# Performance work log

Hardware: AMD Instinct MI355X
Metric: run time of the kernel (lower is better)

The kernel has to match this reference:

```python
import jax, jax.numpy as jnp
import numpy as np

B, S, D = 2, 2048, 1024
H = 16
HD = D // H


def setup_inputs() -> dict:
    key = jax.random.key(0)
    k1, k2, k3 = jax.random.split(key, 3)
    x = jax.random.normal(k1, (B, S, D), dtype=jnp.float32)
    # nn.Linear(d, 3d, bias=False): weight [3d, d]; y = x @ W.T
    w_qkv = jax.random.normal(k2, (3 * D, D), dtype=jnp.float32) * (D ** -0.5)
    w_out = jax.random.normal(k3, (D, D), dtype=jnp.float32) * (D ** -0.5)
    return {"x": x, "w_qkv": w_qkv, "w_out": w_out}


def reference(x, w_qkv, w_out):
    batch, seq_len, _ = x.shape
    qkv = jnp.einsum('bsd,ed->bse', x, w_qkv)  # [B,S,3D]
    q, k, v = jnp.split(qkv, 3, axis=-1)
    # [B,S,D] -> [B,H,S,HD]
    def heads(t):
        return t.reshape(batch, seq_len, H, HD).transpose(0, 2, 1, 3)
    q, k, v = heads(q), heads(k), heads(v)
    scale = HD ** -0.5
    attn = jnp.einsum('bhqd,bhkd->bhqk', q, k) * scale  # [B,H,S,S]
    causal = jnp.triu(jnp.ones((seq_len, seq_len), dtype=bool), k=1)
    attn = jnp.where(causal, -jnp.inf, attn)
    attn = jax.nn.softmax(attn, axis=-1)
    out = jnp.einsum('bhqk,bhkd->bhqd', attn, v)  # [B,H,S,HD]
    out = out.transpose(0, 2, 1, 3).reshape(batch, seq_len, D)
    return jnp.einsum('bsd,ed->bse', out, w_out)
```

## Files before the change

### kernel.cpp

```cpp
#include <hip/hip_runtime.h>

#define NUM_B 2
#define SEQ   2048
#define DIM   1024
#define NH    16
#define HD    64

typedef __attribute__((ext_vector_type(8))) short short8;
typedef __attribute__((ext_vector_type(4))) float floatx4;
typedef unsigned short us;

#define SOFTMAX_SHIFT 12.0f

__device__ __forceinline__ us f2bf(float f) {
    unsigned u = __float_as_uint(f);
    u += 0x7fffu + ((u >> 16) & 1u);
    return (us)(u >> 16);
}
__device__ __forceinline__ us f2bf_t(float f) {
    return (us)(__float_as_uint(f) >> 16);
}

#define GLD16(gptr, lptr) __builtin_amdgcn_global_load_lds( \
    (__attribute__((address_space(1))) unsigned int*)(gptr), \
    (__attribute__((address_space(3))) unsigned int*)(lptr), 16, 0, 0)

#define SETP(p) __builtin_amdgcn_s_setprio(p)

__global__ __launch_bounds__(256) void cast_all(
    const float* __restrict__ x, const float* __restrict__ wq,
    const float* __restrict__ wo, us* __restrict__ xb,
    us* __restrict__ wqb, us* __restrict__ wob)
{
    int i = blockIdx.x * 256 + threadIdx.x;
    const float* src; us* dst; int off;
    if (i < 524288)      { src = x;  dst = xb;  off = i; }
    else if (i < 917504) { src = wq; dst = wqb; off = i - 524288; }
    else                 { src = wo; dst = wob; off = i - 917504; }
    const float4* p = (const float4*)src + (size_t)off * 2;
    float4 f0 = p[0];
    float4 f1 = p[1];
    short8 v;
    v[0] = (short)f2bf(f0.x); v[1] = (short)f2bf(f0.y);
    v[2] = (short)f2bf(f0.z); v[3] = (short)f2bf(f0.w);
    v[4] = (short)f2bf(f1.x); v[5] = (short)f2bf(f1.y);
    v[6] = (short)f2bf(f1.z); v[7] = (short)f2bf(f1.w);
    *(short8*)(dst + (size_t)off * 8) = v;
}

__global__ __launch_bounds__(256, 2) void gemm_qkv(
    const us* __restrict__ A, const us* __restrict__ Bw,
    us* __restrict__ qb, us* __restrict__ kb, us* __restrict__ vt)
{
    __shared__ us As[128 * 64];
    __shared__ us Bs[128 * 64];
    const int t = threadIdx.x;
    const int lane = t & 63, w = t >> 6;
    const int l16 = lane & 15, quad = lane >> 4;
    const int wr = (w >> 1) * 64, wc = (w & 1) * 64;
    const int m0 = blockIdx.y * 128, n0 = blockIdx.x * 128;
    const bool isV = (blockIdx.x >= 16);
    const int srow = lane >> 3;
    const int soff = ((lane & 7) ^ srow) << 3;
    const int rsw  = l16 & 7;

    floatx4 acc[4][4];
    #pragma unroll
    for (int i = 0; i < 4; ++i)
        #pragma unroll
        for (int j = 0; j < 4; ++j) acc[i][j] = (floatx4){0.f, 0.f, 0.f, 0.f};

    for (int k0 = 0; k0 < DIM; k0 += 64) {
        #pragma unroll
        for (int c = 0; c < 4; ++c) {
            int chunk = w * 4 + c;
            int row = chunk * 8 + srow;
            GLD16(A  + (size_t)(m0 + row) * DIM + k0 + soff, &As[chunk * 512]);
            GLD16(Bw + (size_t)(n0 + row) * DIM + k0 + soff, &Bs[chunk * 512]);
        }
        __syncthreads();
        #pragma unroll
        for (int s = 0; s < 2; ++s) {
            short8 af[4], bf[4];
            #pragma unroll
            for (int i = 0; i < 4; ++i)
                af[i] = *(const short8*)&As[(wr + i * 16 + l16) * 64 + (((s * 4 + quad) ^ rsw) << 3)];
            #pragma unroll
            for (int j = 0; j < 4; ++j)
                bf[j] = *(const short8*)&Bs[(wc + j * 16 + l16) * 64 + (((s * 4 + quad) ^ rsw) << 3)];
            if (!isV) {
                #pragma unroll
                for (int i = 0; i < 4; ++i)
                    #pragma unroll
                    for (int j = 0; j < 4; ++j)
                        acc[i][j] = __builtin_amdgcn_mfma_f32_16x16x32_bf16(af[i], bf[j], acc[i][j], 0, 0, 0);
            } else {
                #pragma unroll
                for (int i = 0; i < 4; ++i)
                    #pragma unroll
                    for (int j = 0; j < 4; ++j)
                        acc[i][j] = __builtin_amdgcn_mfma_f32_16x16x32_bf16(bf[j], af[i], acc[i][j], 0, 0, 0);
            }
        }
        __syncthreads();
    }

    if (!isV) {
        const int which = n0 >> 10;
        const float sc = (which == 0) ? 0.125f : 1.0f;
        us* dst = (which == 0) ? qb : kb;
        #pragma unroll
        for (int i = 0; i < 4; ++i) {
            #pragma unroll
            for (int j = 0; j < 4; ++j) {
                int e = n0 + wc + j * 16 + l16;
                int h  = (e >> 6) & 15;
                int hd = e & 63;
                #pragma unroll
                for (int r = 0; r < 4; ++r) {
                    int m = m0 + wr + i * 16 + quad * 4 + r;
                    int b = m >> 11, s = m & 2047;
                    dst[((size_t)((b * NH + h) * SEQ + s) << 6) + hd] = f2bf(acc[i][j][r] * sc);
                }
            }
        }
    } else {
        #pragma unroll
        for (int i = 0; i < 4; ++i) {
            int m = m0 + wr + i * 16 + l16;
            int b = m >> 11, s = m & 2047;
            #pragma unroll
            for (int j = 0; j < 4; ++j) {
                int e0 = (n0 - 2048) + wc + j * 16 + quad * 4;
                #pragma unroll
                for (int r = 0; r < 4; ++r) {
                    int e = e0 + r;
                    int h = e >> 6, hd = e & 63;
                    vt[((size_t)((b * NH + h) * HD + hd) << 11) + s] = f2bf(acc[i][j][r]);
                }
            }
        }
    }
}

__global__ __launch_bounds__(256, 2) void gemm_out(
    const us* __restrict__ A, const us* __restrict__ Bw, float* __restrict__ outp)
{
    __shared__ us As[64 * 64];
    __shared__ us Bs[128 * 64];
    const int t = threadIdx.x;
    const int lane = t & 63, w = t >> 6;
    const int l16 = lane & 15, quad = lane >> 4;
    const int wr = (w >> 1) * 32, wc = (w & 1) * 64;
    const int m0 = blockIdx.y * 64, n0 = blockIdx.x * 128;
    const int srow = lane >> 3;
    const int soff = ((lane & 7) ^ srow) << 3;
    const int rsw  = l16 & 7;

    floatx4 acc[2][4];
    #pragma unroll
    for (int i = 0; i < 2; ++i)
        #pragma unroll
        for (int j = 0; j < 4; ++j) acc[i][j] = (floatx4){0.f, 0.f, 0.f, 0.f};

    for (int k0 = 0; k0 < DIM; k0 += 64) {
        #pragma unroll
        for (int c = 0; c < 2; ++c) {
            int chunk = w * 2 + c;
            int row = chunk * 8 + srow;
            GLD16(A + (size_t)(m0 + row) * DIM + k0 + soff, &As[chunk * 512]);
        }
        #pragma unroll
        for (int c = 0; c < 4; ++c) {
            int chunk = w * 4 + c;
            int row = chunk * 8 + srow;
            GLD16(Bw + (size_t)(n0 + row) * DIM + k0 + soff, &Bs[chunk * 512]);
        }
        __syncthreads();
        #pragma unroll
        for (int s = 0; s < 2; ++s) {
            short8 af[2], bf[4];
            #pragma unroll
            for (int i = 0; i < 2; ++i)
                af[i] = *(const short8*)&As[(wr + i * 16 + l16) * 64 + (((s * 4 + quad) ^ rsw) << 3)];
            #pragma unroll
            for (int j = 0; j < 4; ++j)
                bf[j] = *(const short8*)&Bs[(wc + j * 16 + l16) * 64 + (((s * 4 + quad) ^ rsw) << 3)];
            #pragma unroll
            for (int i = 0; i < 2; ++i)
                #pragma unroll
                for (int j = 0; j < 4; ++j)
                    acc[i][j] = __builtin_amdgcn_mfma_f32_16x16x32_bf16(af[i], bf[j], acc[i][j], 0, 0, 0);
        }
        __syncthreads();
    }

    #pragma unroll
    for (int i = 0; i < 2; ++i)
        #pragma unroll
        for (int j = 0; j < 4; ++j) {
            int n = n0 + wc + j * 16 + l16;
            #pragma unroll
            for (int r = 0; r < 4; ++r) {
                int m = m0 + wr + i * 16 + quad * 4 + r;
                outp[(size_t)m * DIM + n] = acc[i][j][r];
            }
        }
}

__global__ __launch_bounds__(256, 4) void attn(
    const us* __restrict__ qb, const us* __restrict__ kb,
    const us* __restrict__ vt, us* __restrict__ ob)
{
    __shared__ us Ks[2][64 * 64];
    __shared__ us Vs[2][64 * 64];
    __shared__ us Ps[4 * 16 * 72];
    const int t = threadIdx.x;
    const int lane = t & 63, w = t >> 6;
    const int l16 = lane & 15, quad = lane >> 4;
    const int idx = blockIdx.x;
    const int xcd   = idx & 7;
    const int local = idx >> 3;
    const int bh = (xcd << 2) | (local & 3);
    const int qt = 31 - (local >> 2);
    const int b = bh >> 4, h = bh & 15;
    const int q0 = qt << 6;
    const int r0 = q0 + w * 16;
    const int rowb = r0 + quad * 4;
    const size_t base = (size_t)bh * SEQ * HD;
    const us* qbh = qb + base;
    const us* kbh = kb + base;
    const us* vth = vt + base;
    us* Pp = Ps + w * 16 * 72;
    const int srow = lane >> 3;
    const int soff = ((lane & 7) ^ srow) << 3;
    const int rsw  = l16 & 7;

    short8 qa[2];
    #pragma unroll
    for (int s = 0; s < 2; ++s)
        qa[s] = *(const short8*)(qbh + (size_t)(r0 + l16) * HD + s * 32 + quad * 8);

    floatx4 o[4];
    #pragma unroll
    for (int j = 0; j < 4; ++j) o[j] = (floatx4){0.f, 0.f, 0.f, 0.f};
    float lrow[4] = {0.f, 0.f, 0.f, 0.f};

    #pragma unroll
    for (int c = 0; c < 2; ++c) {
        int chunk = w * 2 + c;
        int row = chunk * 8 + srow;
        GLD16(kbh + (size_t)row * HD + soff, &Ks[0][chunk * 512]);
        GLD16(vth + (size_t)row * SEQ + soff, &Vs[0][chunk * 512]);
    }
    __syncthreads();

    for (int kt = 0; kt <= qt; ++kt) {
        const int cur = kt & 1;
        if (kt < qt) {
            const int j0n = (kt + 1) << 6;
            #pragma unroll
            for (int c = 0; c < 2; ++c) {
                int chunk = w * 2 + c;
                int row = chunk * 8 + srow;
                GLD16(kbh + (size_t)(j0n + row) * HD + soff, &Ks[cur ^ 1][chunk * 512]);
                GLD16(vth + (size_t)row * SEQ + j0n + soff, &Vs[cur ^ 1][chunk * 512]);
            }
        }

        floatx4 sf[4];
        #pragma unroll
        for (int j = 0; j < 4; ++j)
            sf[j] = (floatx4){-SOFTMAX_SHIFT, -SOFTMAX_SHIFT, -SOFTMAX_SHIFT, -SOFTMAX_SHIFT};
        SETP(1);
        #pragma unroll
        for (int s = 0; s < 2; ++s)
            #pragma unroll
            for (int j = 0; j < 4; ++j) {
                short8 kf = *(const short8*)&Ks[cur][(j * 16 + l16) * 64 + (((s * 4 + quad) ^ rsw) << 3)];
                sf[j] = __builtin_amdgcn_mfma_f32_16x16x32_bf16(qa[s], kf, sf[j], 0, 0, 0);
            }
        SETP(0);

        float p[4][4];
        #pragma unroll
        for (int j = 0; j < 4; ++j)
            #pragma unroll
            for (int r = 0; r < 4; ++r) p[j][r] = sf[j][r];

        if (kt == qt) {
            const int j0 = kt << 6;
            #pragma unroll
            for (int j = 0; j < 4; ++j) {
                int colg = j0 + j * 16 + l16;
                #pragma unroll
                for (int r = 0; r < 4; ++r)
                    if (colg > rowb + r) p[j][r] = -1e30f;
            }
        }

        #pragma unroll
        for (int j = 0; j < 4; ++j)
            #pragma unroll
            for (int r = 0; r < 4; ++r) {
                p[j][r] = __expf(p[j][r]);
                Pp[(quad * 4 + r) * 72 + j * 16 + l16] = f2bf_t(p[j][r]);
            }
        #pragma unroll
        for (int r = 0; r < 4; ++r)
            lrow[r] += (p[0][r] + p[1][r]) + (p[2][r] + p[3][r]);

        SETP(1);
        #pragma unroll
        for (int s = 0; s < 2; ++s) {
            short8 pf = *(const short8*)&Pp[l16 * 72 + s * 32 + quad * 8];
            #pragma unroll
            for (int j = 0; j < 4; ++j) {
                short8 vf = *(const short8*)&Vs[cur][(j * 16 + l16) * 64 + (((s * 4 + quad) ^ rsw) << 3)];
                o[j] = __builtin_amdgcn_mfma_f32_16x16x32_bf16(pf, vf, o[j], 0, 0, 0);
            }
        }
        SETP(0);
        __syncthreads();
    }

    #pragma unroll
    for (int r = 0; r < 4; ++r) {
        float l = lrow[r];
        l += __shfl_xor(l, 1);
        l += __shfl_xor(l, 2);
        l += __shfl_xor(l, 4);
        l += __shfl_xor(l, 8);
        float inv = 1.0f / l;
        #pragma unroll
        for (int j = 0; j < 4; ++j) {
            float val = o[j][r] * inv;
            ob[(size_t)(b * SEQ + rowb + r) * DIM + h * HD + j * 16 + l16] = f2bf(val);
        }
    }
}

extern "C" void kernel_launch(void* const* d_in, const int* in_sizes, int n_in,
                              void* d_out, int out_size, void* d_ws, size_t ws_size,
                              hipStream_t stream) {
    const float* x     = (const float*)d_in[0];
    const float* w_qkv = (const float*)d_in[1];
    const float* w_out = (const float*)d_in[2];
    float* out = (float*)d_out;
    us* ws = (us*)d_ws;

    const size_t M1 = (size_t)1024 * 1024;
    us* xb  = ws;
    us* wqb = xb  + 4 * M1;
    us* wob = wqb + 3 * M1;
    us* qb  = wob + 1 * M1;
    us* kb  = qb  + 4 * M1;
    us* vt  = kb  + 4 * M1;
    us* obf = vt  + 4 * M1;

    cast_all<<<4096, 256, 0, stream>>>(x, w_qkv, w_out, xb, wqb, wob);
    gemm_qkv<<<dim3(24, 32), 256, 0, stream>>>(xb, wqb, qb, kb, vt);
    attn<<<1024, 256, 0, stream>>>(qb, kb, vt, obf);
    gemm_out<<<dim3(8, 64), 256, 0, stream>>>(obf, wob, out);
}
```

Measured before the change: 169.8 us.

## Enlarge attention query tile to 128 and output GEMM tile to 128x128

The attention kernel now gives each block 128 query rows, with 32 rows per wave, so every K/V tile loaded into shared memory is reused across twice as many queries. Waves whose rows lie entirely above the causal diagonal skip the compute for that key tile. The output projection GEMM moves from 64x128 to 128x128 tiles to improve operand reuse. The cost is half as many blocks in each kernel, more registers per thread (attention launch bounds drop to 2 blocks per SM), and idle waves on the diagonal tiles, which together risk lower occupancy and worse load balance.

```diff
diff --git a/kernel.cpp b/kernel.cpp
--- a/kernel.cpp
+++ b/kernel.cpp
@@ -146,48 +146,43 @@
 __global__ __launch_bounds__(256, 2) void gemm_out(
     const us* __restrict__ A, const us* __restrict__ Bw, float* __restrict__ outp)
 {
-    __shared__ us As[64 * 64];
+    __shared__ us As[128 * 64];
     __shared__ us Bs[128 * 64];
     const int t = threadIdx.x;
     const int lane = t & 63, w = t >> 6;
     const int l16 = lane & 15, quad = lane >> 4;
-    const int wr = (w >> 1) * 32, wc = (w & 1) * 64;
-    const int m0 = blockIdx.y * 64, n0 = blockIdx.x * 128;
+    const int wr = (w >> 1) * 64, wc = (w & 1) * 64;
+    const int m0 = blockIdx.y * 128, n0 = blockIdx.x * 128;
     const int srow = lane >> 3;
     const int soff = ((lane & 7) ^ srow) << 3;
     const int rsw  = l16 & 7;
 
-    floatx4 acc[2][4];
-    #pragma unroll
-    for (int i = 0; i < 2; ++i)
+    floatx4 acc[4][4];
+    #pragma unroll
+    for (int i = 0; i < 4; ++i)
         #pragma unroll
         for (int j = 0; j < 4; ++j) acc[i][j] = (floatx4){0.f, 0.f, 0.f, 0.f};
 
     for (int k0 = 0; k0 < DIM; k0 += 64) {
-        #pragma unroll
-        for (int c = 0; c < 2; ++c) {
-            int chunk = w * 2 + c;
-            int row = chunk * 8 + srow;
-            GLD16(A + (size_t)(m0 + row) * DIM + k0 + soff, &As[chunk * 512]);
-        }
         #pragma unroll
         for (int c = 0; c < 4; ++c) {
             int chunk = w * 4 + c;
             int row = chunk * 8 + srow;
+            GLD16(A  + (size_t)(m0 + row) * DIM + k0 + soff, &As[chunk * 512]);
             GLD16(Bw + (size_t)(n0 + row) * DIM + k0 + soff, &Bs[chunk * 512]);
         }
         __syncthreads();
         #pragma unroll
         for (int s = 0; s < 2; ++s) {
-            short8 af[2], bf[4];
-            #pragma unroll
-            for (int i = 0; i < 2; ++i)
+            short8 af[4], bf[4];
+            #pragma unroll
+            for (int i = 0; i < 4; ++i)
                 af[i] = *(const short8*)&As[(wr + i * 16 + l16) * 64 + (((s * 4 + quad) ^ rsw) << 3)];
             #pragma unroll
             for (int j = 0; j < 4; ++j)
                 bf[j] = *(const short8*)&Bs[(wc + j * 16 + l16) * 64 + (((s * 4 + quad) ^ rsw) << 3)];
             #pragma unroll
-            for (int i = 0; i < 2; ++i)
+            for (int i = 0; i < 4; ++i)
                 #pragma unroll
                 for (int j = 0; j < 4; ++j)
                     acc[i][j] = __builtin_amdgcn_mfma_f32_16x16x32_bf16(af[i], bf[j], acc[i][j], 0, 0, 0);
@@ -196,7 +191,7 @@
     }
 
     #pragma unroll
-    for (int i = 0; i < 2; ++i)
+    for (int i = 0; i < 4; ++i)
         #pragma unroll
         for (int j = 0; j < 4; ++j) {
             int n = n0 + wc + j * 16 + l16;
@@ -208,13 +203,13 @@
         }
 }
 
-__global__ __launch_bounds__(256, 4) void attn(
+__global__ __launch_bounds__(256, 2) void attn(
     const us* __restrict__ qb, const us* __restrict__ kb,
     const us* __restrict__ vt, us* __restrict__ ob)
 {
     __shared__ us Ks[2][64 * 64];
     __shared__ us Vs[2][64 * 64];
-    __shared__ us Ps[4 * 16 * 72];
+    __shared__ us Ps[4 * 32 * 72];
     const int t = threadIdx.x;
     const int lane = t & 63, w = t >> 6;
     const int l16 = lane & 15, quad = lane >> 4;
@@ -222,29 +217,32 @@
     const int xcd   = idx & 7;
     const int local = idx >> 3;
     const int bh = (xcd << 2) | (local & 3);
-    const int qt = 31 - (local >> 2);
+    const int qt = 15 - (local >> 2);
     const int b = bh >> 4, h = bh & 15;
-    const int q0 = qt << 6;
-    const int r0 = q0 + w * 16;
-    const int rowb = r0 + quad * 4;
+    const int q0 = qt << 7;
+    const int r0 = q0 + w * 32;
     const size_t base = (size_t)bh * SEQ * HD;
     const us* qbh = qb + base;
     const us* kbh = kb + base;
     const us* vth = vt + base;
-    us* Pp = Ps + w * 16 * 72;
+    us* Pp = Ps + w * 32 * 72;
     const int srow = lane >> 3;
     const int soff = ((lane & 7) ^ srow) << 3;
     const int rsw  = l16 & 7;
 
-    short8 qa[2];
-    #pragma unroll
-    for (int s = 0; s < 2; ++s)
-        qa[s] = *(const short8*)(qbh + (size_t)(r0 + l16) * HD + s * 32 + quad * 8);
-
-    floatx4 o[4];
-    #pragma unroll
-    for (int j = 0; j < 4; ++j) o[j] = (floatx4){0.f, 0.f, 0.f, 0.f};
-    float lrow[4] = {0.f, 0.f, 0.f, 0.f};
+    short8 qa[2][2];
+    #pragma unroll
+    for (int i = 0; i < 2; ++i)
+        #pragma unroll
+        for (int s = 0; s < 2; ++s)
+            qa[i][s] = *(const short8*)(qbh + (size_t)(r0 + i * 16 + l16) * HD + s * 32 + quad * 8);
+
+    floatx4 o[2][4];
+    float lrow[2][4];
+    #pragma unroll
+    for (int i = 0; i < 2; ++i)
+        #pragma unroll
+        for (int j = 0; j < 4; ++j) { o[i][j] = (floatx4){0.f, 0.f, 0.f, 0.f}; lrow[i][j] = 0.f; }
 
     #pragma unroll
     for (int c = 0; c < 2; ++c) {
@@ -255,9 +253,10 @@
     }
     __syncthreads();
 
-    for (int kt = 0; kt <= qt; ++kt) {
+    const int ktmax = (q0 + 127) >> 6;
+    for (int kt = 0; kt <= ktmax; ++kt) {
         const int cur = kt & 1;
-        if (kt < qt) {
+        if (kt < ktmax) {
             const int j0n = (kt + 1) << 6;
             #pragma unroll
             for (int c = 0; c < 2; ++c) {
@@ -268,74 +267,82 @@
             }
         }
 
-        floatx4 sf[4];
-        #pragma unroll
-        for (int j = 0; j < 4; ++j)
-            sf[j] = (floatx4){-SOFTMAX_SHIFT, -SOFTMAX_SHIFT, -SOFTMAX_SHIFT, -SOFTMAX_SHIFT};
-        SETP(1);
-        #pragma unroll
-        for (int s = 0; s < 2; ++s)
+        if ((kt << 6) <= r0 + 31) {
+            floatx4 sf[2][4];
+            #pragma unroll
+            for (int i = 0; i < 2; ++i)
+                #pragma unroll
+                for (int j = 0; j < 4; ++j)
+                    sf[i][j] = (floatx4){-SOFTMAX_SHIFT, -SOFTMAX_SHIFT, -SOFTMAX_SHIFT, -SOFTMAX_SHIFT};
+            SETP(1);
+            #pragma unroll
+            for (int s = 0; s < 2; ++s)
+                #pragma unroll
+                for (int j = 0; j < 4; ++j) {
+                    short8 kf = *(const short8*)&Ks[cur][(j * 16 + l16) * 64 + (((s * 4 + quad) ^ rsw) << 3)];
+                    #pragma unroll
+                    for (int i = 0; i < 2; ++i)
+                        sf[i][j] = __builtin_amdgcn_mfma_f32_16x16x32_bf16(qa[i][s], kf, sf[i][j], 0, 0, 0);
+                }
+            SETP(0);
+
+            const bool diag = ((kt << 6) + 63 > r0);
+            #pragma unroll
+            for (int i = 0; i < 2; ++i) {
+                const int rowb = r0 + i * 16 + quad * 4;
+                #pragma unroll
+                for (int j = 0; j < 4; ++j) {
+                    int colg = (kt << 6) + j * 16 + l16;
+                    float ps[4];
+                    #pragma unroll
+                    for (int r = 0; r < 4; ++r) {
+                        float v = sf[i][j][r];
+                        if (diag && colg > rowb + r) v = -1e30f;
+                        ps[r] = __expf(v);
+                        Pp[(i * 16 + quad * 4 + r) * 72 + j * 16 + l16] = f2bf_t(ps[r]);
+                    }
+                    lrow[i][0] += ps[0]; lrow[i][1] += ps[1];
+                    lrow[i][2] += ps[2]; lrow[i][3] += ps[3];
+                }
+            }
+
+            short8 pf[2][2];
+            #pragma unroll
+            for (int i = 0; i < 2; ++i)
+                #pragma unroll
+                for (int s = 0; s < 2; ++s)
+                    pf[i][s] = *(const short8*)&Pp[(i * 16 + l16) * 72 + s * 32 + quad * 8];
+            SETP(1);
+            #pragma unroll
+            for (int s = 0; s < 2; ++s)
+                #pragma unroll
+                for (int j = 0; j < 4; ++j) {
+                    short8 vf = *(const short8*)&Vs[cur][(j * 16 + l16) * 64 + (((s * 4 + quad) ^ rsw) << 3)];
+                    #pragma unroll
+                    for (int i = 0; i < 2; ++i)
+                        o[i][j] = __builtin_amdgcn_mfma_f32_16x16x32_bf16(pf[i][s], vf, o[i][j], 0, 0, 0);
+                }
+            SETP(0);
+        }
+        __syncthreads();
+    }
+
+    #pragma unroll
+    for (int i = 0; i < 2; ++i) {
+        const int rowb = r0 + i * 16 + quad * 4;
+        #pragma unroll
+        for (int r = 0; r < 4; ++r) {
+            float l = lrow[i][r];
+            l += __shfl_xor(l, 1);
+            l += __shfl_xor(l, 2);
+            l += __shfl_xor(l, 4);
+            l += __shfl_xor(l, 8);
+            float inv = 1.0f / l;
             #pragma unroll
             for (int j = 0; j < 4; ++j) {
-                short8 kf = *(const short8*)&Ks[cur][(j * 16 + l16) * 64 + (((s * 4 + quad) ^ rsw) << 3)];
-                sf[j] = __builtin_amdgcn_mfma_f32_16x16x32_bf16(qa[s], kf, sf[j], 0, 0, 0);
-            }
-        SETP(0);
-
-        float p[4][4];
-        #pragma unroll
-        for (int j = 0; j < 4; ++j)
-            #pragma unroll
-            for (int r = 0; r < 4; ++r) p[j][r] = sf[j][r];
-
-        if (kt == qt) {
-            const int j0 = kt << 6;
-            #pragma unroll
-            for (int j = 0; j < 4; ++j) {
-                int colg = j0 + j * 16 + l16;
-                #pragma unroll
-                for (int r = 0; r < 4; ++r)
-                    if (colg > rowb + r) p[j][r] = -1e30f;
-            }
-        }
-
-        #pragma unroll
-        for (int j = 0; j < 4; ++j)
-            #pragma unroll
-            for (int r = 0; r < 4; ++r) {
-                p[j][r] = __expf(p[j][r]);
-                Pp[(quad * 4 + r) * 72 + j * 16 + l16] = f2bf_t(p[j][r]);
-            }
-        #pragma unroll
-        for (int r = 0; r < 4; ++r)
-            lrow[r] += (p[0][r] + p[1][r]) + (p[2][r] + p[3][r]);
-
-        SETP(1);
-        #pragma unroll
-        for (int s = 0; s < 2; ++s) {
-            short8 pf = *(const short8*)&Pp[l16 * 72 + s * 32 + quad * 8];
-            #pragma unroll
-            for (int j = 0; j < 4; ++j) {
-                short8 vf = *(const short8*)&Vs[cur][(j * 16 + l16) * 64 + (((s * 4 + quad) ^ rsw) << 3)];
-                o[j] = __builtin_amdgcn_mfma_f32_16x16x32_bf16(pf, vf, o[j], 0, 0, 0);
-            }
-        }
-        SETP(0);
-        __syncthreads();
-    }
-
-    #pragma unroll
-    for (int r = 0; r < 4; ++r) {
-        float l = lrow[r];
-        l += __shfl_xor(l, 1);
-        l += __shfl_xor(l, 2);
-        l += __shfl_xor(l, 4);
-        l += __shfl_xor(l, 8);
-        float inv = 1.0f / l;
-        #pragma unroll
-        for (int j = 0; j < 4; ++j) {
-            float val = o[j][r] * inv;
-            ob[(size_t)(b * SEQ + rowb + r) * DIM + h * HD + j * 16 + l16] = f2bf(val);
+                float val = o[i][j][r] * inv;
+                ob[(size_t)(b * SEQ + rowb + r) * DIM + h * HD + j * 16 + l16] = f2bf(val);
+            }
         }
     }
 }
@@ -360,6 +367,6 @@
 
     cast_all<<<4096, 256, 0, stream>>>(x, w_qkv, w_out, xb, wqb, wob);
     gemm_qkv<<<dim3(24, 32), 256, 0, stream>>>(xb, wqb, qb, kb, vt);
-    attn<<<1024, 256, 0, stream>>>(qb, kb, vt, obf);
-    gemm_out<<<dim3(8, 64), 256, 0, stream>>>(obf, wob, out);
-}
+    attn<<<512, 256, 0, stream>>>(qb, kb, vt, obf);
+    gemm_out<<<dim3(8, 32), 256, 0, stream>>>(obf, wob, out);
+}
```

Result: slower. 191.3 us (+12.7%).
